# Optimization experiments

Hardware: AMD Instinct MI355X
Metric: run time of the kernel (lower is better)

The kernel has to match this reference:

```python
import jax, jax.numpy as jnp
import numpy as np

N_NODES = 20000
N_EDGES = 160000
FEAT = 512
HEADS = 4
NEG_SLOPE = 0.2


def setup_inputs() -> dict:
    key = jax.random.key(0)
    ks = jax.random.split(key, 8)
    s = 1.0 / np.sqrt(FEAT)
    return {
        "x": jax.random.normal(ks[0], (N_NODES, FEAT), dtype=jnp.float32),
        "edge_index": jax.random.randint(ks[1], (2, N_EDGES), 0, N_NODES, dtype=jnp.int32),
        "W_l": jax.random.normal(ks[2], (FEAT, HEADS * FEAT), dtype=jnp.float32) * s,
        "W_r": jax.random.normal(ks[3], (FEAT, HEADS * FEAT), dtype=jnp.float32) * s,
        "att": jax.random.normal(ks[4], (HEADS, FEAT), dtype=jnp.float32) * s,
        "bias": jax.random.normal(ks[5], (FEAT,), dtype=jnp.float32) * 0.01,
        "W_cls": jax.random.normal(ks[6], (FEAT, 2), dtype=jnp.float32) * s,
        "b_cls": jnp.zeros((2,), dtype=jnp.float32),
    }


def reference(x, edge_index, W_l, W_r, att, bias, W_cls, b_cls):
    N = x.shape[0]
    H, C = att.shape
    # PyG GATv2Conv default: add self-loops
    loops = jnp.arange(N, dtype=edge_index.dtype)
    ei = jnp.concatenate([edge_index, jnp.stack([loops, loops])], axis=1)
    src, dst = ei[0], ei[1]  # message j -> i

    xl = (x @ W_l).reshape(N, H, C)  # source transform
    xr = (x @ W_r).reshape(N, H, C)  # target transform

    # GATv2 score: e_ij = att . LeakyReLU(xl_j + xr_i)   -> [E, H]
    u = xl[src] + xr[dst]                      # [E, H, C]
    e = jnp.einsum('ehc,hc->eh', jax.nn.leaky_relu(u, NEG_SLOPE), att)

    # segment softmax over incoming edges of each dst node
    m = jax.ops.segment_max(e, dst, num_segments=N)          # [N, H]
    alpha = jnp.exp(e - m[dst])
    denom = jax.ops.segment_sum(alpha, dst, num_segments=N)  # [N, H]
    alpha = alpha / denom[dst]

    # aggregate: out_i = sum_j alpha_ij * xl_j
    out = jax.ops.segment_sum(alpha[:, :, None] * xl[src], dst, num_segments=N)  # [N,H,C]
    out = out.mean(axis=1) + bias  # concat=False -> mean over heads, then bias

    return out @ W_cls + b_cls  # [N, num_classes]
```

## Files before the change

kernel.cpp:

```cpp
#include <hip/hip_runtime.h>
#include <hip/hip_bf16.h>

#define FEAT    512
#define HEADS   4
#define NEG     0.2f

typedef unsigned int uint;
typedef unsigned short ushort_t;
typedef __attribute__((ext_vector_type(8))) short bf16x8v;
typedef __attribute__((ext_vector_type(4))) float f32x4v;
typedef __attribute__((address_space(3))) uint lds_u32_t;
typedef __attribute__((address_space(1))) const uint g_u32_t;

__device__ inline float bf2f(ushort_t h) { return __uint_as_float(((uint)h) << 16); }
__device__ inline ushort_t f2bf(float f) {
    uint u = __float_as_uint(f);
    u += 0x7fff + ((u >> 16) & 1);
    return (ushort_t)(u >> 16);
}
__device__ inline float2 up2(uint d) {
    return make_float2(__uint_as_float(d << 16), __uint_as_float(d & 0xffff0000u));
}
__device__ inline float2 f2add(float2 a, float2 b) { return make_float2(a.x + b.x, a.y + b.y); }
__device__ inline float2 f2min0(float2 a) { return make_float2(fminf(a.x, 0.f), fminf(a.y, 0.f)); }
__device__ inline float2 f2fma(float2 a, float2 b, float2 c) {
    return make_float2(fmaf(a.x, b.x, c.x), fmaf(a.y, b.y, c.y));
}
__device__ inline float2 f2fmas(float s, float2 b, float2 c) {
    return make_float2(fmaf(s, b.x, c.x), fmaf(s, b.y, c.y));
}

__global__ void probe_dtype(const ushort_t* __restrict__ x, int* flag) {
    int lane = threadIdx.x;
    int hits = 0;
    for (int i = lane; i < 128; i += 64) {
        ushort_t w = x[2 * i];
        uint hb = (w >> 8) & 0x7f;
        hits += (hb >= 0x38 && hb <= 0x42) ? 1 : 0;
    }
    #pragma unroll
    for (int off = 32; off >= 1; off >>= 1) hits += __shfl_xor(hits, off);
    if (lane == 0) *flag = (hits >= 64) ? 1 : 0;
}

__global__ __launch_bounds__(256) void canon_kernel(const void* __restrict__ in,
                                                    ushort_t* __restrict__ outp,
                                                    const int* __restrict__ flag, long long n,
                                                    int skip_if_bf16) {
    int isbf = *flag;
    if (isbf && skip_if_bf16) return;
    long long i0 = ((long long)blockIdx.x * 256 + threadIdx.x) * 8;
    if (i0 + 8 <= n) {
        if (isbf) {
            *(uint4*)&outp[i0] = *(const uint4*)((const ushort_t*)in + i0);
        } else {
            const float* f = (const float*)in + i0;
            float4 a = *(const float4*)f, b = *(const float4*)(f + 4);
            ushort_t o[8] = {f2bf(a.x), f2bf(a.y), f2bf(a.z), f2bf(a.w),
                             f2bf(b.x), f2bf(b.y), f2bf(b.z), f2bf(b.w)};
            *(uint4*)&outp[i0] = *(uint4*)o;
        }
    } else {
        for (long long i = i0; i < n; ++i)
            outp[i] = isbf ? ((const ushort_t*)in)[i] : f2bf(((const float*)in)[i]);
    }
}

__global__ void hist_kernel(const int* __restrict__ dst, int* deg, int E, int N) {
    int i = blockIdx.x * blockDim.x + threadIdx.x;
    if (i < E) {
        int d = dst[i];
        if ((uint)d < (uint)N) atomicAdd(&deg[d], 1);
    }
}

__global__ __launch_bounds__(256) void scan1(const int* __restrict__ deg, int* __restrict__ part,
                                             int* __restrict__ bsum, int N) {
    __shared__ int tmp[256];
    int b = blockIdx.x, tid = threadIdx.x;
    int i0 = b * 1024 + tid * 4;
    int v[4] = {0, 0, 0, 0};
    if (i0 + 4 <= N) { int4 q = *(const int4*)&deg[i0]; v[0]=q.x+1; v[1]=q.y+1; v[2]=q.z+1; v[3]=q.w+1; }
    else { for (int j = 0; j < 4; ++j) v[j] = (i0 + j < N) ? deg[i0 + j] + 1 : 0; }
    int s0 = v[0], s1 = s0 + v[1], s2 = s1 + v[2], s3 = s2 + v[3];
    tmp[tid] = s3;
    __syncthreads();
    for (int off = 1; off < 256; off <<= 1) {
        int t = (tid >= off) ? tmp[tid - off] : 0;
        __syncthreads();
        tmp[tid] += t;
        __syncthreads();
    }
    int base = tid ? tmp[tid - 1] : 0;
    int e[4] = {base, base + s0, base + s1, base + s2};
    if (i0 + 4 <= N) { *(int4*)&part[i0] = make_int4(e[0], e[1], e[2], e[3]); }
    else { for (int j = 0; j < 4; ++j) if (i0 + j < N) part[i0 + j] = e[j]; }
    if (tid == 255) bsum[b] = tmp[255];
}

__global__ void scan2(int* __restrict__ bsum, int* __restrict__ offsN, int Nb) {
    int lane = threadIdx.x;
    int carry = 0;
    for (int base = 0; base < Nb; base += 64) {
        int idx = base + lane;
        int v = (idx < Nb) ? bsum[idx] : 0;
        int incl = v;
        #pragma unroll
        for (int off = 1; off < 64; off <<= 1) {
            int t = __shfl_up(incl, off);
            if (lane >= off) incl += t;
        }
        if (idx < Nb) bsum[idx] = carry + (incl - v);
        carry += __shfl(incl, 63);
    }
    if (lane == 0) *offsN = carry;
}

__global__ __launch_bounds__(256) void scan3(const int* __restrict__ part, const int* __restrict__ bsum,
                                             int* __restrict__ offsets, int* __restrict__ cursor, int N) {
    int b = blockIdx.x;
    int add = bsum[b];
    int i0 = b * 1024 + threadIdx.x * 4;
    #pragma unroll
    for (int j = 0; j < 4; ++j) {
        int i = i0 + j;
        if (i < N) { int o = part[i] + add; offsets[i] = o; cursor[i] = o; }
    }
}

__global__ void scatter_kernel(const int* __restrict__ src, const int* __restrict__ dst,
                               int* cursor, int* srcs, int E, int N) {
    int i = blockIdx.x * blockDim.x + threadIdx.x;
    if (i >= E + N) return;
    int s, d;
    if (i < E) { s = src[i]; d = dst[i]; }
    else       { s = i - E; d = i - E; }
    if ((uint)d >= (uint)N) return;
    int pos = atomicAdd(&cursor[d], 1);
    if ((uint)pos < (uint)(E + N)) srcs[pos] = s;
}

__global__ __launch_bounds__(256) void transpose_canon(const void* __restrict__ in,
                                                       ushort_t* __restrict__ outp,
                                                       const int* __restrict__ flag,
                                                       int K, int N) {
    __shared__ ushort_t t[64][72];
    int k0 = blockIdx.y * 64, n0 = blockIdx.x * 64;
    int tid = threadIdx.x;
    int r = tid >> 3;
    int c = (tid & 7) * 8;
    int isbf = *flag;
    #pragma unroll
    for (int p = 0; p < 2; ++p) {
        int row = r + p * 32;
        size_t base = (size_t)(k0 + row) * N + n0 + c;
        if (isbf) {
            *(uint4*)&t[row][c] = *(const uint4*)((const ushort_t*)in + base);
        } else {
            const float* f = (const float*)in + base;
            float4 a = *(const float4*)f, b = *(const float4*)(f + 4);
            ushort_t o[8] = {f2bf(a.x), f2bf(a.y), f2bf(a.z), f2bf(a.w),
                             f2bf(b.x), f2bf(b.y), f2bf(b.z), f2bf(b.w)};
            *(uint4*)&t[row][c] = *(uint4*)o;
        }
    }
    __syncthreads();
    #pragma unroll
    for (int p = 0; p < 2; ++p) {
        int row = r + p * 32;
        #pragma unroll
        for (int j = 0; j < 8; ++j)
            outp[(size_t)(n0 + row) * K + k0 + c + j] = t[c + j][row];
    }
}

__global__ __launch_bounds__(256) void gemm128(const ushort_t* A_bf, const ushort_t* A_cv,
                                               const int* __restrict__ flag,
                                               const ushort_t* __restrict__ Bt,
                                               ushort_t* __restrict__ C,
                                               int M, int Nn, int K) {
    __shared__ ushort_t As[2][128 * 32];
    __shared__ ushort_t Bs[2][128 * 32];
    const ushort_t* A = (*flag) ? A_bf : A_cv;
    int tid = threadIdx.x;
    int wave = tid >> 6, lane = tid & 63;
    int row0 = blockIdx.y * 128, col0 = blockIdx.x * 128;
    int wm = (wave >> 1) * 64, wn = (wave & 1) * 64;

    f32x4v acc[4][4];
    #pragma unroll
    for (int i = 0; i < 4; ++i)
        #pragma unroll
        for (int j = 0; j < 4; ++j) acc[i][j] = (f32x4v){0.f, 0.f, 0.f, 0.f};

    int fm = lane & 15, kq8 = (lane >> 4) * 8;

    const ushort_t* srcA[2]; ushort_t* dstA0[2]; ushort_t* dstA1[2];
    const ushort_t* srcB[2]; ushort_t* dstB0[2]; ushort_t* dstB1[2];
    #pragma unroll
    for (int i = 0; i < 2; ++i) {
        int p = (wave * 2 + i) * 64 + lane;
        int row = p >> 2, kp = p & 3;
        int gra = row0 + row; if (gra >= M) gra = M - 1;
        srcA[i] = &A[(size_t)gra * K + kp * 8];
        srcB[i] = &Bt[(size_t)(col0 + row) * K + kp * 8];
        dstA0[i] = &As[0][p * 8]; dstA1[i] = &As[1][p * 8];
        dstB0[i] = &Bs[0][p * 8]; dstB1[i] = &Bs[1][p * 8];
    }

    for (int k0 = 0; k0 < K; k0 += 64) {
        #pragma unroll
        for (int i = 0; i < 2; ++i) {
            __builtin_amdgcn_global_load_lds((g_u32_t*)srcA[i],        (lds_u32_t*)dstA0[i], 16, 0, 0);
            __builtin_amdgcn_global_load_lds((g_u32_t*)(srcA[i] + 32), (lds_u32_t*)dstA1[i], 16, 0, 0);
            __builtin_amdgcn_global_load_lds((g_u32_t*)srcB[i],        (lds_u32_t*)dstB0[i], 16, 0, 0);
            __builtin_amdgcn_global_load_lds((g_u32_t*)(srcB[i] + 32), (lds_u32_t*)dstB1[i], 16, 0, 0);
            srcA[i] += 64; srcB[i] += 64;
        }
        __syncthreads();

        #pragma unroll
        for (int panel = 0; panel < 2; ++panel) {
            bf16x8v af[4], bfr[4];
            #pragma unroll
            for (int mi = 0; mi < 4; ++mi)
                af[mi] = *(const bf16x8v*)&As[panel][(wm + mi * 16 + fm) * 32 + kq8];
            #pragma unroll
            for (int nj = 0; nj < 4; ++nj)
                bfr[nj] = *(const bf16x8v*)&Bs[panel][(wn + nj * 16 + fm) * 32 + kq8];
            #pragma unroll
            for (int mi = 0; mi < 4; ++mi)
                #pragma unroll
                for (int nj = 0; nj < 4; ++nj)
                    acc[mi][nj] = __builtin_amdgcn_mfma_f32_16x16x32_bf16(af[mi], bfr[nj], acc[mi][nj], 0, 0, 0);
        }
        __syncthreads();
    }

    int col = lane & 15, rq = (lane >> 4) * 4;
    #pragma unroll
    for (int mi = 0; mi < 4; ++mi) {
        #pragma unroll
        for (int r = 0; r < 4; ++r) {
            int gm = row0 + wm + mi * 16 + rq + r;
            if (gm < M) {
                #pragma unroll
                for (int nj = 0; nj < 4; ++nj)
                    C[(size_t)gm * Nn + col0 + wn + nj * 16 + col] = f2bf(acc[mi][nj][r]);
            }
        }
    }
}

__global__ __launch_bounds__(256) void gat_aggregate(
    const ushort_t* __restrict__ xl, int xl_stride,
    const ushort_t* __restrict__ xr, int xr_stride,
    const int* __restrict__ offsets, const int* __restrict__ srcs,
    const ushort_t* __restrict__ att, const ushort_t* __restrict__ bias,
    const ushort_t* __restrict__ Wc, const ushort_t* __restrict__ bc,
    float* __restrict__ out, int c0, int Cn, int N, int EN) {
    int bn = blockIdx.x;
    if (bn >= Cn) return;
    int n = c0 + bn;
    int tid = threadIdx.x;
    int h = tid >> 6, lane = tid & 63;
    int hoff = h * FEAT + lane * 8;

    __shared__ float sh[HEADS][FEAT];
    __shared__ float r0s[HEADS], r1s[HEADS];

    float2 xrr[4], attr[4];
    { uint4 q = *(const uint4*)&xr[(size_t)bn * xr_stride + hoff];
      xrr[0] = up2(q.x); xrr[1] = up2(q.y); xrr[2] = up2(q.z); xrr[3] = up2(q.w); }
    { uint4 q = *(const uint4*)&att[hoff];
      attr[0] = up2(q.x); attr[1] = up2(q.y); attr[2] = up2(q.z); attr[3] = up2(q.w); }

    int start = offsets[n], end = offsets[n + 1];
    start = max(0, min(start, EN));
    end   = max(start, min(end, EN));
    int deg = end - start;

    int sv = 0;
    if (lane < deg) sv = srcs[start + lane];

    float l = 0.f;
    float2 acc[4] = {{0.f,0.f},{0.f,0.f},{0.f,0.f},{0.f,0.f}};
    const ushort_t* xlh = xl + hoff;
    const float2 cneg = make_float2(NEG - 1.0f, NEG - 1.0f);

    auto getS = [&](int i) -> int {
        int s = (i < 64) ? __shfl(sv, i) : srcs[start + i];
        return ((uint)s >= (uint)N) ? 0 : s;
    };
    auto body = [&](uint4 q) {
        float2 v[4] = {up2(q.x), up2(q.y), up2(q.z), up2(q.w)};
        float2 p2 = make_float2(0.f, 0.f);
        #pragma unroll
        for (int j = 0; j < 4; ++j) {
            float2 u  = f2add(v[j], xrr[j]);
            float2 lr = f2fma(f2min0(u), cneg, u);
            p2 = f2fma(lr, attr[j], p2);
        }
        float p = p2.x + p2.y;
        #pragma unroll
        for (int off = 32; off >= 1; off >>= 1) p += __shfl_xor(p, off);
        float w = __expf(p);
        l += w;
        #pragma unroll
        for (int j = 0; j < 4; ++j) acc[j] = f2fmas(w, v[j], acc[j]);
    };

    uint4 cur0, cur1;
    {
        int s0 = getS(0);
        int s1 = getS(deg > 1 ? 1 : 0);
        cur0 = *(const uint4*)(xlh + (size_t)s0 * xl_stride);
        cur1 = *(const uint4*)(xlh + (size_t)s1 * xl_stride);
    }
    int e = 0;
    for (; e + 2 < deg; e += 2) {
        int t0 = getS(e + 2);
        int t1 = getS(e + 3 < deg ? e + 3 : e + 2);
        uint4 n0 = *(const uint4*)(xlh + (size_t)t0 * xl_stride);
        uint4 n1 = *(const uint4*)(xlh + (size_t)t1 * xl_stride);
        body(cur0);
        body(cur1);
        cur0 = n0; cur1 = n1;
    }
    body(cur0);
    if (deg - e == 2) body(cur1);

    float inv = 0.25f / fmaxf(l, 1e-35f);
    #pragma unroll
    for (int j = 0; j < 4; ++j) {
        sh[h][lane * 8 + 2 * j]     = acc[j].x * inv;
        sh[h][lane * 8 + 2 * j + 1] = acc[j].y * inv;
    }
    __syncthreads();

    float p0 = 0.f, p1 = 0.f;
    for (int c = tid; c < FEAT; c += 256) {
        float f = sh[0][c] + sh[1][c] + sh[2][c] + sh[3][c] + bf2f(bias[c]);
        uint w2 = *(const uint*)&Wc[c * 2];
        p0 = fmaf(f, bf2f((ushort_t)(w2 & 0xffff)), p0);
        p1 = fmaf(f, bf2f((ushort_t)(w2 >> 16)), p1);
    }
    #pragma unroll
    for (int off = 32; off >= 1; off >>= 1) {
        p0 += __shfl_xor(p0, off);
        p1 += __shfl_xor(p1, off);
    }
    if (lane == 0) { r0s[h] = p0; r1s[h] = p1; }
    __syncthreads();
    if (tid == 0) {
        out[(size_t)n * 2 + 0] = r0s[0] + r0s[1] + r0s[2] + r0s[3] + bf2f(bc[0]);
        out[(size_t)n * 2 + 1] = r1s[0] + r1s[1] + r1s[2] + r1s[3] + bf2f(bc[1]);
    }
}

extern "C" void kernel_launch(void* const* d_in, const int* in_sizes, int n_in,
                              void* d_out, int out_size, void* d_ws, size_t ws_size,
                              hipStream_t stream) {
    const void* x    = d_in[0];
    const int*  ei   = (const int*)d_in[1];
    const void* W_l  = d_in[2];
    const void* W_r  = d_in[3];
    const void* att  = d_in[4];
    const void* bias = d_in[5];
    const void* Wc   = d_in[6];
    const void* bc   = d_in[7];
    float* out = (float*)d_out;

    const int N  = in_sizes[0] / FEAT;
    const int E  = in_sizes[1] / 2;
    const int K  = FEAT;
    const int HC = HEADS * FEAT;
    const int EN = E + N;
    const int Nb = (N + 1023) / 1024;

    const int* src = ei;
    const int* dst = ei + E;

    char* base = (char*)d_ws;
    size_t off = 0;
    auto alloc = [&](size_t bytes) -> char* {
        char* p = base + off;
        off = (off + bytes + 255) & ~(size_t)255;
        return p;
    };
    int* flag    = (int*)alloc(4);
    int* offsets = (int*)alloc((size_t)(N + 1) * 4);
    int* cursor  = (int*)alloc((size_t)N * 4);
    int* deg     = (int*)alloc((size_t)N * 4);
    int* part    = (int*)alloc((size_t)N * 4);
    int* bsum    = (int*)alloc((size_t)(Nb + 1) * 4);
    int* srcs    = (int*)alloc((size_t)EN * 4);
    ushort_t* attc  = (ushort_t*)alloc((size_t)HC * 2);
    ushort_t* biasc = (ushort_t*)alloc((size_t)FEAT * 2);
    ushort_t* Wcc   = (ushort_t*)alloc((size_t)FEAT * 2 * 2);
    ushort_t* bcc   = (ushort_t*)alloc(2 * 2);
    ushort_t* xc   = (ushort_t*)alloc((size_t)N * K * 2);
    ushort_t* Wcat = (ushort_t*)alloc((size_t)2 * HC * K * 2);
    size_t fixed = off;

    size_t need_merged = (size_t)N * 2 * HC * 2;
    bool merged = (ws_size >= fixed + need_merged);

    probe_dtype<<<1, 64, 0, stream>>>((const ushort_t*)x, flag);
    long long NX = (long long)N * K;
    canon_kernel<<<(int)((NX + 2047) / 2048), 256, 0, stream>>>(x, xc, flag, NX, 1);
    canon_kernel<<<1, 256, 0, stream>>>(att, attc, flag, HC, 0);
    canon_kernel<<<1, 256, 0, stream>>>(bias, biasc, flag, FEAT, 0);
    canon_kernel<<<1, 256, 0, stream>>>(Wc, Wcc, flag, FEAT * 2, 0);
    canon_kernel<<<1, 256, 0, stream>>>(bc, bcc, flag, 2, 0);

    hipMemsetAsync(deg, 0, (size_t)N * 4, stream);
    hist_kernel<<<(E + 255) / 256, 256, 0, stream>>>(dst, deg, E, N);
    scan1<<<Nb, 256, 0, stream>>>(deg, part, bsum, N);
    scan2<<<1, 64, 0, stream>>>(bsum, &offsets[N], Nb);
    scan3<<<Nb, 256, 0, stream>>>(part, bsum, offsets, cursor, N);
    scatter_kernel<<<(EN + 255) / 256, 256, 0, stream>>>(src, dst, cursor, srcs, E, N);

    dim3 tg(HC / 64, K / 64);
    transpose_canon<<<tg, 256, 0, stream>>>(W_l, Wcat, flag, K, HC);
    transpose_canon<<<tg, 256, 0, stream>>>(W_r, Wcat + (size_t)HC * K, flag, K, HC);

    const ushort_t* x_bf = (const ushort_t*)x;

    if (merged) {
        ushort_t* xlr = (ushort_t*)(base + fixed);
        dim3 gg(2 * HC / 128, (N + 127) / 128);
        gemm128<<<gg, 256, 0, stream>>>(x_bf, xc, flag, Wcat, xlr, N, 2 * HC, K);
        gat_aggregate<<<N, 256, 0, stream>>>(xlr, 2 * HC, xlr + HC, 2 * HC,
                                             offsets, srcs, attc, biasc, Wcc, bcc,
                                             out, 0, N, N, EN);
    } else {
        ushort_t* xl = (ushort_t*)alloc((size_t)N * HC * 2);
        size_t remain = (ws_size > off) ? (ws_size - off) : 0;
        long long Cmax = (long long)(remain / ((size_t)HC * 2));
        int C = (Cmax >= N) ? N : (int)(Cmax & ~63LL);
        if (C < 64) C = 64;
        ushort_t* xrc = (ushort_t*)(base + off);
        ushort_t* Wlt = Wcat;
        ushort_t* Wrt = Wcat + (size_t)HC * K;

        dim3 gl(HC / 128, (N + 127) / 128);
        gemm128<<<gl, 256, 0, stream>>>(x_bf, xc, flag, Wlt, xl, N, HC, K);
        for (int c0 = 0; c0 < N; c0 += C) {
            int Cn = (N - c0 < C) ? (N - c0) : C;
            dim3 gr(HC / 128, (Cn + 127) / 128);
            gemm128<<<gr, 256, 0, stream>>>(x_bf + (size_t)c0 * K, xc + (size_t)c0 * K, flag,
                                            Wrt, xrc, Cn, HC, K);
            gat_aggregate<<<Cn, 256, 0, stream>>>(xl, HC, xrc, HC,
                                                  offsets, srcs, attc, biasc, Wcc, bcc,
                                                  out, c0, Cn, N, EN);
        }
    }
}
```

Measured before the change: 353.9 us.

## Double-buffer GEMM k-loop, deepen gather prefetch, merge small canon launches

The GEMM main loop now prefetches the next 32-wide K slice into the other LDS buffer while computing on the current one, with one barrier per iteration instead of loading both panels and then computing. The attention-aggregation loop prefetches two edge pairs ahead with clamped indices instead of one, to hide more gather latency. The four tiny canonicalization launches become a single kernel. This overlaps load and compute in exchange for more syncs per K and extra clamped loads at the tail of each edge list.

```diff
diff --git a/kernel.cpp b/kernel.cpp
--- a/kernel.cpp
+++ b/kernel.cpp
@@ -66,6 +66,26 @@
     }
 }
 
+__global__ __launch_bounds__(256) void canon_small4(
+    const void* a0, ushort_t* o0, int n0, const void* a1, ushort_t* o1, int n1,
+    const void* a2, ushort_t* o2, int n2, const void* a3, ushort_t* o3, int n3,
+    const int* __restrict__ flag) {
+    int isbf = *flag;
+    int idx = blockIdx.x * 256 + threadIdx.x;
+    const void* srcs[4] = {a0, a1, a2, a3};
+    ushort_t* dsts[4] = {o0, o1, o2, o3};
+    int ns[4] = {n0, n1, n2, n3};
+    #pragma unroll
+    for (int k = 0; k < 4; ++k) {
+        if (idx < ns[k]) {
+            dsts[k][idx] = isbf ? ((const ushort_t*)srcs[k])[idx]
+                                : f2bf(((const float*)srcs[k])[idx]);
+            return;
+        }
+        idx -= ns[k];
+    }
+}
+
 __global__ void hist_kernel(const int* __restrict__ dst, int* deg, int E, int N) {
     int i = blockIdx.x * blockDim.x + threadIdx.x;
     if (i < E) {
@@ -195,8 +215,8 @@
 
     int fm = lane & 15, kq8 = (lane >> 4) * 8;
 
-    const ushort_t* srcA[2]; ushort_t* dstA0[2]; ushort_t* dstA1[2];
-    const ushort_t* srcB[2]; ushort_t* dstB0[2]; ushort_t* dstB1[2];
+    const ushort_t* srcA[2]; ushort_t* dstA[2][2];
+    const ushort_t* srcB[2]; ushort_t* dstB[2][2];
     #pragma unroll
     for (int i = 0; i < 2; ++i) {
         int p = (wave * 2 + i) * 64 + lane;
@@ -204,36 +224,41 @@
         int gra = row0 + row; if (gra >= M) gra = M - 1;
         srcA[i] = &A[(size_t)gra * K + kp * 8];
         srcB[i] = &Bt[(size_t)(col0 + row) * K + kp * 8];
-        dstA0[i] = &As[0][p * 8]; dstA1[i] = &As[1][p * 8];
-        dstB0[i] = &Bs[0][p * 8]; dstB1[i] = &Bs[1][p * 8];
-    }
-
-    for (int k0 = 0; k0 < K; k0 += 64) {
-        #pragma unroll
-        for (int i = 0; i < 2; ++i) {
-            __builtin_amdgcn_global_load_lds((g_u32_t*)srcA[i],        (lds_u32_t*)dstA0[i], 16, 0, 0);
-            __builtin_amdgcn_global_load_lds((g_u32_t*)(srcA[i] + 32), (lds_u32_t*)dstA1[i], 16, 0, 0);
-            __builtin_amdgcn_global_load_lds((g_u32_t*)srcB[i],        (lds_u32_t*)dstB0[i], 16, 0, 0);
-            __builtin_amdgcn_global_load_lds((g_u32_t*)(srcB[i] + 32), (lds_u32_t*)dstB1[i], 16, 0, 0);
-            srcA[i] += 64; srcB[i] += 64;
-        }
-        __syncthreads();
-
-        #pragma unroll
-        for (int panel = 0; panel < 2; ++panel) {
-            bf16x8v af[4], bfr[4];
+        dstA[0][i] = &As[0][p * 8]; dstA[1][i] = &As[1][p * 8];
+        dstB[0][i] = &Bs[0][p * 8]; dstB[1][i] = &Bs[1][p * 8];
+    }
+
+    #pragma unroll
+    for (int i = 0; i < 2; ++i) {
+        __builtin_amdgcn_global_load_lds((g_u32_t*)srcA[i], (lds_u32_t*)dstA[0][i], 16, 0, 0);
+        __builtin_amdgcn_global_load_lds((g_u32_t*)srcB[i], (lds_u32_t*)dstB[0][i], 16, 0, 0);
+        srcA[i] += 32; srcB[i] += 32;
+    }
+    __syncthreads();
+
+    int nIter = K >> 5;
+    for (int it = 0; it < nIter; ++it) {
+        int cur = it & 1, nxt = cur ^ 1;
+        if (it + 1 < nIter) {
             #pragma unroll
-            for (int mi = 0; mi < 4; ++mi)
-                af[mi] = *(const bf16x8v*)&As[panel][(wm + mi * 16 + fm) * 32 + kq8];
+            for (int i = 0; i < 2; ++i) {
+                __builtin_amdgcn_global_load_lds((g_u32_t*)srcA[i], (lds_u32_t*)dstA[nxt][i], 16, 0, 0);
+                __builtin_amdgcn_global_load_lds((g_u32_t*)srcB[i], (lds_u32_t*)dstB[nxt][i], 16, 0, 0);
+                srcA[i] += 32; srcB[i] += 32;
+            }
+        }
+        bf16x8v af[4], bfr[4];
+        #pragma unroll
+        for (int mi = 0; mi < 4; ++mi)
+            af[mi] = *(const bf16x8v*)&As[cur][(wm + mi * 16 + fm) * 32 + kq8];
+        #pragma unroll
+        for (int nj = 0; nj < 4; ++nj)
+            bfr[nj] = *(const bf16x8v*)&Bs[cur][(wn + nj * 16 + fm) * 32 + kq8];
+        #pragma unroll
+        for (int mi = 0; mi < 4; ++mi)
             #pragma unroll
             for (int nj = 0; nj < 4; ++nj)
-                bfr[nj] = *(const bf16x8v*)&Bs[panel][(wn + nj * 16 + fm) * 32 + kq8];
-            #pragma unroll
-            for (int mi = 0; mi < 4; ++mi)
-                #pragma unroll
-                for (int nj = 0; nj < 4; ++nj)
-                    acc[mi][nj] = __builtin_amdgcn_mfma_f32_16x16x32_bf16(af[mi], bfr[nj], acc[mi][nj], 0, 0, 0);
-        }
+                acc[mi][nj] = __builtin_amdgcn_mfma_f32_16x16x32_bf16(af[mi], bfr[nj], acc[mi][nj], 0, 0, 0);
         __syncthreads();
     }
 
@@ -289,8 +314,16 @@
     const float2 cneg = make_float2(NEG - 1.0f, NEG - 1.0f);
 
     auto getS = [&](int i) -> int {
+        if (i < 0) i = 0;
+        if (i >= deg) i = deg - 1;
+        if (i < 0) i = 0;
         int s = (i < 64) ? __shfl(sv, i) : srcs[start + i];
         return ((uint)s >= (uint)N) ? 0 : s;
+    };
+    auto fetchPair = [&](int i0, uint4& q0, uint4& q1) {
+        int s0 = getS(i0), s1 = getS(i0 + 1);
+        q0 = *(const uint4*)(xlh + (size_t)s0 * xl_stride);
+        q1 = *(const uint4*)(xlh + (size_t)s1 * xl_stride);
     };
     auto body = [&](uint4 q) {
         float2 v[4] = {up2(q.x), up2(q.y), up2(q.z), up2(q.w)};
@@ -310,25 +343,15 @@
         for (int j = 0; j < 4; ++j) acc[j] = f2fmas(w, v[j], acc[j]);
     };
 
-    uint4 cur0, cur1;
-    {
-        int s0 = getS(0);
-        int s1 = getS(deg > 1 ? 1 : 0);
-        cur0 = *(const uint4*)(xlh + (size_t)s0 * xl_stride);
-        cur1 = *(const uint4*)(xlh + (size_t)s1 * xl_stride);
-    }
-    int e = 0;
-    for (; e + 2 < deg; e += 2) {
-        int t0 = getS(e + 2);
-        int t1 = getS(e + 3 < deg ? e + 3 : e + 2);
-        uint4 n0 = *(const uint4*)(xlh + (size_t)t0 * xl_stride);
-        uint4 n1 = *(const uint4*)(xlh + (size_t)t1 * xl_stride);
-        body(cur0);
-        body(cur1);
-        cur0 = n0; cur1 = n1;
-    }
-    body(cur0);
-    if (deg - e == 2) body(cur1);
+    uint4 a0, a1, b0, b1, q0, q1;
+    fetchPair(0, a0, a1);
+    fetchPair(2, b0, b1);
+    for (int e = 0; e < deg; e += 2) {
+        fetchPair(e + 4, q0, q1);
+        body(a0);
+        if (e + 1 < deg) body(a1);
+        a0 = b0; a1 = b1; b0 = q0; b1 = q1;
+    }
 
     float inv = 0.25f / fmaxf(l, 1e-35f);
     #pragma unroll
@@ -409,10 +432,8 @@
     probe_dtype<<<1, 64, 0, stream>>>((const ushort_t*)x, flag);
     long long NX = (long long)N * K;
     canon_kernel<<<(int)((NX + 2047) / 2048), 256, 0, stream>>>(x, xc, flag, NX, 1);
-    canon_kernel<<<1, 256, 0, stream>>>(att, attc, flag, HC, 0);
-    canon_kernel<<<1, 256, 0, stream>>>(bias, biasc, flag, FEAT, 0);
-    canon_kernel<<<1, 256, 0, stream>>>(Wc, Wcc, flag, FEAT * 2, 0);
-    canon_kernel<<<1, 256, 0, stream>>>(bc, bcc, flag, 2, 0);
+    canon_small4<<<15, 256, 0, stream>>>(att, attc, HC, bias, biasc, FEAT,
+                                         Wc, Wcc, FEAT * 2, bc, bcc, 2, flag);
 
     hipMemsetAsync(deg, 0, (size_t)N * 4, stream);
     hist_kernel<<<(E + 255) / 256, 256, 0, stream>>>(dst, deg, E, N);
```

New measurement: 354.6 us. About the same (+0.2%).
